# Kernel tuning notes

Hardware: AMD Instinct MI355X
Metric: run time of the kernel (lower is better)

The kernel has to match this reference:

```python
import jax, jax.numpy as jnp
import numpy as np

D = 256          # descriptor_dim
H = 4            # num heads in AttentionPropagation
DH = D // H
SCALE = 0.1      # hparams['scale_factor']
THR = 0.2        # hparams['match_threshold']
NAMES = ['GATs', 'self', 'cross'] * 4


def conv1d(x, w, b):
    # 1x1 Conv1d == per-position matmul. x:[b,c,n] w:[o,c] b:[o]
    return jnp.einsum('oc,bcn->bon', w, x) + b[None, :, None]


def instnorm(x, eps=1e-5):
    # torch InstanceNorm1d (affine=False): normalize over spatial dim per channel
    mu = jnp.mean(x, axis=2, keepdims=True)
    var = jnp.var(x, axis=2, keepdims=True)
    return (x - mu) * jax.lax.rsqrt(var + eps)


def linear_attention(q, k, v):
    # q:[b,dh,h,nq] k,v:[b,dh,h,ns]
    eps = 1e-6
    q = jax.nn.elu(q) + 1.0
    k = jax.nn.elu(k) + 1.0
    m = v.shape[3]
    v = v / m
    KV = jnp.einsum('bdhm,bqhm->bqdh', k, v)
    Z = 1.0 / (jnp.einsum('bdhm,bdh->bhm', q, k.sum(3)) + eps)
    return jnp.einsum('bdhm,bqdh,bhm->bqhm', q, KV, Z) * m


def mha(x, src, pw, pb, mw, mb):
    b, _, nq = x.shape
    ns = src.shape[2]
    q = conv1d(x, pw[0], pb[0]).reshape(b, DH, H, nq)
    k = conv1d(src, pw[1], pb[1]).reshape(b, DH, H, ns)
    v = conv1d(src, pw[2], pb[2]).reshape(b, DH, H, ns)
    o = linear_attention(q, k, v).reshape(b, D, nq)
    return conv1d(o, mw, mb)


def attn_prop(x, src, pw, pb, mw, mb, w1, b1, w2, b2):
    msg = mha(x, src, pw, pb, mw, mb)
    y = jnp.concatenate([x, msg], axis=1)           # [b, 2D, n]
    y = jax.nn.relu(instnorm(conv1d(y, w1, b1)))
    return conv1d(y, w2, b2)


def gat(d2d, d3d, W, a):
    # GraphAttentionLayer (OnePose): include_self=True, additional=False,
    # with_linear_transform=True, concat=True; dropout inactive at eval.
    # d2d:[b,D,n*L] d3d:[b,D,n]
    b, _, n = d3d.shape
    x2 = jnp.transpose(d2d, (0, 2, 1)).reshape(b, n, -1, D)   # [b,n,L,D]
    x3 = jnp.transpose(d3d, (0, 2, 1))                        # [b,n,D]
    x2 = jnp.concatenate([x3[:, :, None, :], x2], axis=2)     # include self -> L+1
    Wh2 = jnp.einsum('bnld,do->bnlo', x2, W)
    Wh3 = jnp.einsum('bnd,do->bno', x3, W)
    e = jax.nn.leaky_relu(
        jnp.einsum('bno,o->bn', Wh3, a[:D])[:, :, None]
        + jnp.einsum('bnlo,o->bnl', Wh2, a[D:]), 0.2)
    att = jax.nn.softmax(e, axis=-1)
    h = jnp.einsum('bnl,bnld->bnd', att, Wh2)
    return jnp.transpose(jax.nn.elu(h), (0, 2, 1))            # [b,D,n]


def gnn_and_scores(dq, d3, d2db, projw, projb, mergew, mergeb,
                   mlp1w, mlp1b, mlp2w, mlp2b, gatW, gata, finw, finb):
    gi = 0
    ai = 0
    for name in NAMES:
        if name == 'GATs':
            d3 = gat(d2db, d3, gatW[gi], gata[gi])
            gi += 1
        else:
            src0, src1 = (d3, dq) if name == 'cross' else (dq, d3)
            p = (projw[ai], projb[ai], mergew[ai], mergeb[ai],
                 mlp1w[ai], mlp1b[ai], mlp2w[ai], mlp2b[ai])
            dq = dq + attn_prop(dq, src0, *p)
            d3 = d3 + attn_prop(d3, src1, *p)
            ai += 1
    mq = conv1d(dq, finw, finb)
    md = conv1d(d3, finw, finb)
    mq = mq / jnp.maximum(jnp.linalg.norm(mq, axis=1, keepdims=True), 1e-12)
    md = md / jnp.maximum(jnp.linalg.norm(md, axis=1, keepdims=True), 1e-12)
    scores = jnp.einsum('bdn,bdm->bnm', mq, md) / SCALE
    conf = jax.nn.softmax(scores, axis=1) * jax.nn.softmax(scores, axis=2)
    return conf


def setup_inputs() -> dict:
    key = jax.random.key(0)
    ks = jax.random.split(key, 16)
    b, n1, n2, L = 2, 3072, 3072, 8
    s = 0.02
    f32 = jnp.float32
    return {
        'desc2d_query': jax.random.normal(ks[0], (b, D, n1), f32),
        'desc3d_db': jax.random.normal(ks[1], (b, D, n2), f32),
        'desc2d_db': jax.random.normal(ks[2], (b, D, n2 * L), f32),
        'projw': jax.random.normal(ks[3], (8, 3, D, D), f32) * s,
        'projb': jnp.zeros((8, 3, D), f32),
        'mergew': jax.random.normal(ks[4], (8, D, D), f32) * s,
        'mergeb': jnp.zeros((8, D), f32),
        'mlp1w': jax.random.normal(ks[5], (8, 2 * D, 2 * D), f32) * s,
        'mlp1b': jnp.zeros((8, 2 * D), f32),
        'mlp2w': jax.random.normal(ks[6], (8, D, 2 * D), f32) * s,
        'mlp2b': jnp.zeros((8, D), f32),
        'gatW': jax.random.normal(ks[7], (4, D, D), f32) * s,
        'gata': jax.random.normal(ks[8], (4, 2 * D), f32) * s,
        'finw': jax.random.normal(ks[9], (D, D), f32) * s,
        'finb': jnp.zeros((D,), f32),
    }


def reference(desc2d_query, desc3d_db, desc2d_db, projw, projb, mergew, mergeb,
              mlp1w, mlp1b, mlp2w, mlp2b, gatW, gata, finw, finb):
    conf = gnn_and_scores(desc2d_query, desc3d_db, desc2d_db, projw, projb,
                          mergew, mergeb, mlp1w, mlp1b, mlp2w, mlp2b,
                          gatW, gata, finw, finb)
    b, n1, n2 = conf.shape
    i0 = jnp.argmax(conf, axis=2)
    m0 = jnp.max(conf, axis=2)
    i1 = jnp.argmax(conf, axis=1)
    m1 = jnp.max(conf, axis=1)
    mutual0 = jnp.arange(n1)[None] == jnp.take_along_axis(i1, i0, axis=1)
    mutual1 = jnp.arange(n2)[None] == jnp.take_along_axis(i0, i1, axis=1)
    ms0 = jnp.where(mutual0, m0, 0.0)
    ms1 = jnp.where(mutual1, jnp.take_along_axis(ms0, i1, axis=1), 0.0)
    valid0 = mutual0 & (ms0 > THR)
    valid1 = mutual1 & jnp.take_along_axis(valid0, i1, axis=1)
    ind0 = jnp.where(valid0, i0, -1)
    ind1 = jnp.where(valid1, i1, -1)
    return (ind0[0], ind1[0], ms0[0], ms1[0], conf)
```

## Files before the change

### kernel.cpp

```cpp
#include <hip/hip_runtime.h>
#include <hip/hip_bf16.h>
#include <math.h>

typedef long long ll;
typedef __attribute__((ext_vector_type(8))) short s8v;
typedef __attribute__((ext_vector_type(4))) float f4v;
typedef __attribute__((address_space(1))) unsigned int gu32;
typedef __attribute__((address_space(3))) unsigned int lu32;

#define NPOS 3072

#define OFF_STF   0LL
#define OFF_STB   3145728LL
#define OFF_QKV   4718592LL
#define OFF_MSG   9437184LL
#define OFF_HID   11010048LL
#define OFF_WBF   14155776LL
#define OFF_PBP   16941056LL
#define OFF_UVEC  17026048LL
#define OFF_E2ALL 17028096LL
#define OFF_PMAX  17300480LL
#define OFF_PSUM  17595392LL
#define OFF_CMAX  17890304LL
#define OFF_CSUM  17896448LL
#define OFF_CAPV  17902592LL
#define OFF_CAPI  17976320LL
#define OFF_I0    18050048LL
#define OFF_M0    18053120LL
#define OFF_I1    18056192LL
#define OFF_M1B   18059264LL
#define OFF_B1C   18583552LL
#define OFF_INAT  18587648LL
#define OFF_SVSQ  18620416LL
#define OFF_KVAT  18632704LL
#define OFF_KSAT  19156992LL
#define ZERO_N    577536LL

__device__ __forceinline__ float b2f(short s) {
  union { unsigned u; float f; } c;
  c.u = ((unsigned)(unsigned short)s) << 16;
  return c.f;
}
__device__ __forceinline__ short f2b(float f) {
  __hip_bfloat16 h = __float2bfloat16(f);
  union { __hip_bfloat16 h; short s; } c; c.h = h; return c.s;
}
__device__ __forceinline__ unsigned pk2(float a, float b) {
  return (unsigned)(unsigned short)f2b(a) | ((unsigned)(unsigned short)f2b(b) << 16);
}
__device__ __forceinline__ float waveSum(float v) {
#pragma unroll
  for (int off = 32; off > 0; off >>= 1) v += __shfl_down(v, off);
  return v;
}
__device__ __forceinline__ void gld16(const short* g, short* l) {
  __builtin_amdgcn_global_load_lds((const gu32*)g, (lu32*)l, 16, 0, 0);
}
template<int N> __device__ __forceinline__ void wvm() {
  asm volatile("s_waitcnt vmcnt(%0)" :: "n"(N) : "memory");
}
__device__ __forceinline__ void wlgk0() {
  asm volatile("s_waitcnt lgkmcnt(0)" ::: "memory");
}

template<int BI, int BJ, int KT, int SMODE>
__global__ __launch_bounds__(256) void bgemm_k(
    const short* __restrict__ A, const short* __restrict__ A2, int KS,
    int lda, int lda2,
    const short* __restrict__ B,
    const float* __restrict__ bias, const float* __restrict__ R,
    float* __restrict__ C, short* __restrict__ C2,
    const float* __restrict__ rs, const float* __restrict__ cs,
    int ldc, float alpha,
    ll aB, ll a2B, ll bB, ll rB, ll cB, ll c2B,
    int za, int zbo, int act, int zand,
    float* __restrict__ sp0, float* __restrict__ sp1, int rsmode)
{
  constexpr int NT = KT / 32;
  constexpr int WI = (BI == 128) ? 2 : 1;
  constexpr int JW = BJ / (4 / WI);
  constexpr int FI = (BI / WI) / 16;
  constexpr int FJ = JW / 16;
  constexpr int SA = BI / 64, SB = BJ / 64;
  constexpr int LPT = SA + SB;
  __shared__ __align__(16) short As[3][BI * 32];
  __shared__ __align__(16) short Bs[3][BJ * 32];
  const int z = blockIdx.z;
  const int zA = (z + za) & zand, zB = (z + zbo) & zand;
  const int j0 = blockIdx.x * BJ, i0 = blockIdx.y * BI;
  const int t = threadIdx.x;
  const int lane = t & 63, w = t >> 6;
  const int wi = (WI == 2) ? (w & 1) * 64 : 0;
  const int wj = (WI == 2) ? (w >> 1) * JW : w * JW;
  const int fr = lane & 15;
  const int cl = lane >> 4;
  const int r4 = cl * 4;

  const short* baseA[SA]; const short* baseA2[SA]; const short* baseB[SB];
  int slA[SA], slB[SB];
  {
    const short* Az = A + (ll)zA * aB;
    const short* A2z = A2 ? A2 + (ll)zA * a2B : nullptr;
    const short* Bz = B + (ll)zB * bB;
#pragma unroll
    for (int i = 0; i < SA; ++i) {
      int cc = t + i * 256;
      int r = cc >> 2;
      int sq = ((cc & 3) ^ ((r >> 1) & 3)) << 3;
      baseA[i] = Az + (ll)(i0 + r) * lda + sq;
      baseA2[i] = A2 ? A2z + (ll)(i0 + r) * lda2 + sq : nullptr;
      slA[i] = cc << 3;
    }
#pragma unroll
    for (int i = 0; i < SB; ++i) {
      int cc = t + i * 256;
      int r = cc >> 2;
      int sq = ((cc & 3) ^ ((r >> 1) & 3)) << 3;
      baseB[i] = Bz + (ll)(j0 + r) * KT + sq;
      slB[i] = cc << 3;
    }
  }
  int offA[FI], offB[FJ];
#pragma unroll
  for (int im = 0; im < FI; ++im) {
    int ra = wi + im * 16 + fr;
    offA[im] = ra * 32 + ((cl ^ ((ra >> 1) & 3)) << 3);
  }
#pragma unroll
  for (int in = 0; in < FJ; ++in) {
    int rb = wj + in * 16 + fr;
    offB[in] = rb * 32 + ((cl ^ ((rb >> 1) & 3)) << 3);
  }

  f4v acc[FI][FJ];
#pragma unroll
  for (int i = 0; i < FI; ++i)
#pragma unroll
    for (int j = 0; j < FJ; ++j) acc[i][j] = (f4v)0.f;

  auto stage = [&](int tile, int bi_) {
    const int k0 = tile * 32;
    short* dA = As[bi_]; short* dB = Bs[bi_];
    if (A2 && k0 >= KS) {
#pragma unroll
      for (int i = 0; i < SA; ++i) gld16(baseA2[i] + (k0 - KS), dA + slA[i]);
    } else {
#pragma unroll
      for (int i = 0; i < SA; ++i) gld16(baseA[i] + k0, dA + slA[i]);
    }
#pragma unroll
    for (int i = 0; i < SB; ++i) gld16(baseB[i] + k0, dB + slB[i]);
  };

  stage(0, 0);
  stage(1, 1);
#pragma unroll
  for (int kt = 0; kt < NT; ++kt) {
    if (kt + 2 < NT) { stage(kt + 2, (kt + 2) % 3); wvm<2 * LPT>(); }
    else if (kt + 1 < NT) { wvm<LPT>(); }
    else { wvm<0>(); }
    __builtin_amdgcn_s_barrier();
    asm volatile("" ::: "memory");
    const short* Ac = As[kt % 3]; const short* Bc = Bs[kt % 3];
    s8v af[FI], bfr[FJ];
#pragma unroll
    for (int im = 0; im < FI; ++im) af[im] = *(const s8v*)(Ac + offA[im]);
#pragma unroll
    for (int in = 0; in < FJ; ++in) bfr[in] = *(const s8v*)(Bc + offB[in]);
#pragma unroll
    for (int im = 0; im < FI; ++im)
#pragma unroll
      for (int in = 0; in < FJ; ++in)
        acc[im][in] = __builtin_amdgcn_mfma_f32_16x16x32_bf16(
            af[im], bfr[in], acc[im][in], 0, 0, 0);
    if (kt + 1 < NT) {
      wlgk0();
      __builtin_amdgcn_s_barrier();
    }
  }

  float* Cz = C ? C + (ll)z * cB : nullptr;
  short* C2z = C2 ? C2 + (ll)z * c2B : nullptr;
  const float* Rz = R ? R + (ll)z * rB : nullptr;
  const float* rsz = rs ? rs + (ll)z * NPOS : nullptr;
  float bv4[FJ], cv4[FJ];
#pragma unroll
  for (int in = 0; in < FJ; ++in) {
    int j = j0 + wj + in * 16 + fr;
    bv4[in] = bias ? bias[j] : 0.f;
    cv4[in] = cs ? cs[(ll)zB * NPOS + j] : 1.f;
    if (rsmode) cv4[in] = 1.f / fmaxf(sqrtf(cv4[in]), 1e-12f);
  }
  float stM[FJ], stS[FJ], stQ[FJ];
#pragma unroll
  for (int in = 0; in < FJ; ++in) { stM[in] = -3.4e38f; stS[in] = 0.f; stQ[in] = 0.f; }

#pragma unroll
  for (int im = 0; im < FI; ++im) {
#pragma unroll
    for (int r = 0; r < 4; ++r) {
      int i = i0 + wi + im * 16 + r4 + r;
      float rsv = rsz ? rsz[i] : 1.f;
      if (rsmode) rsv = 1.f / fmaxf(sqrtf(rsv), 1e-12f);
      int rowo = i * ldc;
      float rq3 = 0.f;
#pragma unroll
      for (int in = 0; in < FJ; ++in) {
        int j = j0 + wj + in * 16 + fr;
        float v = acc[im][in][r] * alpha;
        if (rsz) v = v * rsv * cv4[in];
        v += bv4[in];
        int off = rowo + j;
        if (Rz) v += Rz[off];
        if (act) v = v > 0.f ? v : (expf(v) - 1.f);
        if constexpr (SMODE == 1) {
          float m = stM[in];
          if (v > m) { stS[in] = stS[in] * expf(m - v) + 1.f; stM[in] = v; }
          else stS[in] += expf(v - m);
        }
        if constexpr (SMODE == 2) { stS[in] += v; stQ[in] = fmaf(v, v, stQ[in]); }
        if constexpr (SMODE == 3) rq3 = fmaf(v, v, rq3);
        if (Cz) Cz[off] = v;
        if (C2z) C2z[off] = f2b(v);
      }
      if constexpr (SMODE == 3) {
        rq3 += __shfl_xor(rq3, 1);
        rq3 += __shfl_xor(rq3, 2);
        rq3 += __shfl_xor(rq3, 4);
        rq3 += __shfl_xor(rq3, 8);
        if (fr == 0) atomicAdd(&sp0[(ll)z * NPOS + i], rq3);
      }
    }
  }
  if constexpr (SMODE == 1) {
    const ll totj = (ll)gridDim.x * BJ;
#pragma unroll
    for (int in = 0; in < FJ; ++in) {
      float m = stM[in], s = stS[in];
#pragma unroll
      for (int d = 16; d <= 32; d <<= 1) {
        float mo = __shfl_xor(m, d);
        float so = __shfl_xor(s, d);
        float M = fmaxf(m, mo);
        s = s * expf(m - M) + so * expf(mo - M);
        m = M;
      }
      if (cl == 0) {
        ll o = ((ll)z * gridDim.y + blockIdx.y) * totj + (j0 + wj + in * 16 + fr);
        sp0[o] = m; sp1[o] = s;
      }
    }
  }
  if constexpr (SMODE == 2) {
    const ll totj = (ll)gridDim.x * BJ;
#pragma unroll
    for (int in = 0; in < FJ; ++in) {
      float s = stS[in], q = stQ[in];
      s += __shfl_xor(s, 16); s += __shfl_xor(s, 32);
      q += __shfl_xor(q, 16); q += __shfl_xor(q, 32);
      if (cl == 0) {
        ll o = ((ll)z * totj + (j0 + wj + in * 16 + fr)) * 2;
        atomicAdd(&sp0[o], s);
        atomicAdd(&sp0[o + 1], q);
      }
    }
  }
}

__global__ void zero_k(float* __restrict__ p, int n)
{
  int i = blockIdx.x * 1024 + threadIdx.x * 4;
  if (i < n) *(float4*)(p + i) = make_float4(0.f, 0.f, 0.f, 0.f);
}

__global__ void transpose_in_k(const float* __restrict__ dq, const float* __restrict__ d3,
                               float* __restrict__ stf, short* __restrict__ stb)
{
  __shared__ float tile[64][65];
  int z = blockIdx.z;
  const float* src = (z < 2) ? dq + (ll)z * 786432 : d3 + (ll)(z - 2) * 786432;
  int c0 = blockIdx.y * 64, n0 = blockIdx.x * 64;
  int t = threadIdx.x;
  int nj = t & 63, q = t >> 6;
#pragma unroll
  for (int i = 0; i < 16; ++i) {
    int ci = q + i * 4;
    tile[ci][nj] = src[(ll)(c0 + ci) * NPOS + n0 + nj];
  }
  __syncthreads();
  int cj = t & 63;
#pragma unroll
  for (int i = 0; i < 16; ++i) {
    int ni = q + i * 4;
    float v = tile[cj][ni];
    ll o = (ll)z * 786432 + (ll)(n0 + ni) * 256 + c0 + cj;
    stf[o] = v;
    stb[o] = f2b(v);
  }
}

__global__ void f2b_k(const float* __restrict__ src, short* __restrict__ dst, int n8)
{
  int gi = blockIdx.x * 256 + threadIdx.x;
  if (gi >= n8) return;
  ll e = (ll)gi * 8;
  float4 a = *(const float4*)(src + e);
  float4 b = *(const float4*)(src + e + 4);
  uint4 o;
  o.x = pk2(a.x, a.y); o.y = pk2(a.z, a.w);
  o.z = pk2(b.x, b.y); o.w = pk2(b.z, b.w);
  *(uint4*)(dst + e) = o;
}

__global__ void f2b_split_k(const float* __restrict__ src, short* __restrict__ d1,
                            short* __restrict__ d2)
{
  int gi = blockIdx.x * 256 + threadIdx.x;
  ll e = (ll)gi * 8;
  int k = (int)(e & 511);
  ll row = e >> 9;
  float4 a = *(const float4*)(src + e);
  float4 b = *(const float4*)(src + e + 4);
  uint4 o;
  o.x = pk2(a.x, a.y); o.y = pk2(a.z, a.w);
  o.z = pk2(b.x, b.y); o.w = pk2(b.z, b.w);
  if (k < 256) *(uint4*)(d1 + row * 512 + k) = o;
  else         *(uint4*)(d2 + row * 256 + (k - 256)) = o;
}

__global__ void projw_perm_k(const float* __restrict__ src, short* __restrict__ dst)
{
  int idx = blockIdx.x * 256 + threadIdx.x;
  int c = idx & 255;
  int row = (idx >> 8) % 768;
  int ai = (idx >> 8) / 768;
  int sec = row >> 8;
  int p = row & 255;
  int o = (p & 63) * 4 + (p >> 6);
  dst[idx] = f2b(src[(((ll)ai * 3 + sec) * 256 + o) * 256 + c]);
}

__global__ void pbp_k(const float* __restrict__ pb, float* __restrict__ pbp)
{
  int idx = blockIdx.x * 256 + threadIdx.x;
  int row = idx % 768, ai = idx / 768;
  int sec = row >> 8;
  int p = row & 255;
  int o = (p & 63) * 4 + (p >> 6);
  pbp[idx] = pb[ai * 768 + (sec << 8) + o];
}

__global__ void mergewT_k(const float* __restrict__ src, short* __restrict__ dst)
{
  __shared__ float tile[64][65];
  int ai = blockIdx.z;
  int p0 = blockIdx.x * 64, c0 = blockIdx.y * 64;
  int h = p0 >> 6;
  int t = threadIdx.x;
  int q = t & 63, cq = t >> 6;
#pragma unroll
  for (int i = 0; i < 16; ++i) {
    int cc = cq + i * 4;
    tile[q][cc] = src[(ll)ai * 65536 + (ll)(c0 + cc) * 256 + 4 * q + h];
  }
  __syncthreads();
#pragma unroll
  for (int i = 0; i < 16; ++i) {
    int pi = cq + i * 4;
    dst[((ll)ai * 256 + p0 + pi) * 256 + c0 + q] = f2b(tile[pi][q]);
  }
}

__global__ void biasfold_k(const float* __restrict__ mlp1w, const float* __restrict__ mlp1b,
                           const float* __restrict__ mergeb, float* __restrict__ b1c)
{
  int b = blockIdx.x;
  int ai = b >> 3, o0 = (b & 7) * 64;
  int t = threadIdx.x;
  int w = t >> 6, lane = t & 63;
  float4 mb = *(const float4*)(mergeb + ai * 256 + lane * 4);
#pragma unroll
  for (int ol = 0; ol < 16; ++ol) {
    int o = o0 + w * 16 + ol;
    float4 wv = *(const float4*)(mlp1w + ((ll)(ai * 512 + o)) * 512 + 256 + lane * 4);
    float s = wv.x * mb.x + wv.y * mb.y + wv.z * mb.z + wv.w * mb.w;
    s = waveSum(s);
    if (lane == 0) b1c[ai * 512 + o] = mlp1b[ai * 512 + o] + s;
  }
}

__global__ void gatw_t_k(const float* __restrict__ src, short* __restrict__ dst)
{
  __shared__ float tile[64][65];
  int gi = blockIdx.z;
  int d0 = blockIdx.x * 64, o0 = blockIdx.y * 64;
  int t = threadIdx.x;
  int nj = t & 63, q = t >> 6;
#pragma unroll
  for (int i = 0; i < 16; ++i) {
    int di = q + i * 4;
    tile[di][nj] = src[(ll)gi * 65536 + (ll)(d0 + di) * 256 + o0 + nj];
  }
  __syncthreads();
#pragma unroll
  for (int i = 0; i < 16; ++i) {
    int oi = q + i * 4;
    dst[(ll)gi * 65536 + (ll)(o0 + oi) * 256 + d0 + nj] = f2b(tile[nj][oi]);
  }
}

__global__ void gat_prep_k(const float* __restrict__ gatW, const float* __restrict__ gata,
                           float* __restrict__ uvec)
{
  int gi = blockIdx.x; int d = threadIdx.x;
  const float* W = gatW + (ll)gi * 65536;
  const float* a = gata + gi * 512;
  float u0 = 0.f, u1 = 0.f;
  for (int o = 0; o < 256; o += 4) {
    float4 w4 = *(const float4*)(W + d * 256 + o);
    float4 a4 = *(const float4*)(a + o);
    float4 b4 = *(const float4*)(a + 256 + o);
    u0 += w4.x * a4.x + w4.y * a4.y + w4.z * a4.z + w4.w * a4.w;
    u1 += w4.x * b4.x + w4.y * b4.y + w4.z * b4.z + w4.w * b4.w;
  }
  uvec[gi * 512 + d] = u0;
  uvec[gi * 512 + 256 + d] = u1;
}

__global__ void e2all_k(const float* __restrict__ d2db, const float* __restrict__ uvec,
                        float* __restrict__ e2all)
{
  __shared__ float us[1024];
  int t = threadIdx.x;
  for (int idx = t; idx < 1024; idx += 256)
    us[idx] = uvec[(idx >> 8) * 512 + 256 + (idx & 255)];
  __syncthreads();
  int m = blockIdx.x * 256 + t;
  int b = blockIdx.y;
  const float* xb = d2db + (ll)b * 6291456;
  float a[4] = {};
  for (int c = 0; c < 256; ++c) {
    float v = xb[(ll)c * 24576 + m];
#pragma unroll
    for (int g = 0; g < 4; ++g) a[g] = fmaf(v, us[g * 256 + c], a[g]);
  }
#pragma unroll
  for (int g = 0; g < 4; ++g) e2all[((ll)g * 2 + b) * 24576 + m] = a[g];
}

__global__ __launch_bounds__(256) void gat_g_k(
    const short* __restrict__ stb, const float* __restrict__ d2db,
    const float* __restrict__ uvec, const float* __restrict__ e2all,
    short* __restrict__ g, int gi)
{
  __shared__ float ush[512];
  __shared__ float attw[576];
  __shared__ float gtile[64 * 69];
  const int n0 = blockIdx.x * 64, c0 = blockIdx.y * 64, b = blockIdx.z;
  const int t = threadIdx.x;
  for (int idx = t; idx < 512; idx += 256) ush[idx] = uvec[gi * 512 + idx];
  __syncthreads();
  {
    const int q = t & 3, pl = t >> 2;
    const int n = n0 + pl;
    const short* xr = stb + (ll)(2 + b) * 786432 + (ll)n * 256 + q * 64;
    float a0 = 0.f, a1 = 0.f;
#pragma unroll
    for (int i = 0; i < 8; ++i) {
      s8v v8 = *(const s8v*)(xr + i * 8);
#pragma unroll
      for (int j = 0; j < 8; ++j) {
        float v = b2f(v8[j]);
        a0 = fmaf(v, ush[q * 64 + i * 8 + j], a0);
        a1 = fmaf(v, ush[256 + q * 64 + i * 8 + j], a1);
      }
    }
    a0 += __shfl_xor(a0, 1); a0 += __shfl_xor(a0, 2);
    a1 += __shfl_xor(a1, 1); a1 += __shfl_xor(a1, 2);
    if (q == 0) {
      float e[9];
      e[0] = a0 + a1;
      const float* e2b = e2all + ((ll)gi * 2 + b) * 24576 + (ll)n * 8;
#pragma unroll
      for (int l = 0; l < 8; ++l) e[l + 1] = a0 + e2b[l];
      float mx = -3.4e38f;
#pragma unroll
      for (int l = 0; l < 9; ++l) {
        e[l] = e[l] >= 0.f ? e[l] : 0.2f * e[l];
        mx = fmaxf(mx, e[l]);
      }
      float s = 0.f;
#pragma unroll
      for (int l = 0; l < 9; ++l) { e[l] = expf(e[l] - mx); s += e[l]; }
      float inv = 1.f / s;
#pragma unroll
      for (int l = 0; l < 9; ++l) attw[pl * 9 + l] = e[l] * inv;
    }
  }
  __syncthreads();
  const int nl = t >> 2, l2 = (t & 3) * 2;
  for (int cc = 0; cc < 64; ++cc) {
    const float* src = d2db + ((ll)b * 256 + c0 + cc) * 24576 + (ll)n0 * 8;
    float2 v = *(const float2*)(src + t * 2);
    float p = v.x * attw[nl * 9 + 1 + l2] + v.y * attw[nl * 9 + 2 + l2];
    p += __shfl_xor(p, 1);
    p += __shfl_xor(p, 2);
    if ((t & 3) == 0) gtile[nl * 69 + cc] = p;
  }
  __syncthreads();
#pragma unroll
  for (int i = 0; i < 4; ++i) {
    int n = (t >> 4) + i * 16;
    int cp = (t & 15) * 4;
    float at0 = attw[n * 9];
    const short* dr = stb + (ll)(2 + b) * 786432 + (ll)(n0 + n) * 256 + c0 + cp;
    uint2 dv = *(const uint2*)dr;
    float d0 = b2f((short)(dv.x & 0xffff)), d1 = b2f((short)(dv.x >> 16));
    float d2 = b2f((short)(dv.y & 0xffff)), d3v = b2f((short)(dv.y >> 16));
    uint2 ov;
    ov.x = pk2(gtile[n * 69 + cp] + at0 * d0, gtile[n * 69 + cp + 1] + at0 * d1);
    ov.y = pk2(gtile[n * 69 + cp + 2] + at0 * d2, gtile[n * 69 + cp + 3] + at0 * d3v);
    *(uint2*)(g + (ll)b * 786432 + (ll)(n0 + n) * 256 + c0 + cp) = ov;
  }
}

__global__ __launch_bounds__(256) void kv_partial_k(
    const short* __restrict__ qkv, float* __restrict__ kvat, float* __restrict__ ksat)
{
  __shared__ float ks[32][66];
  __shared__ float vs[32][66];
  const int p = blockIdx.x, h = blockIdx.y, z = blockIdx.z;
  const short* base = qkv + (ll)z * 2359296;
  const int t = threadIdx.x;
  const int tq = (t >> 4) * 4, tk = (t & 15) * 4;
  const int ml = t >> 3, d8 = (t & 7) * 8;
  float acc[4][4] = {};
  float ksl = 0.f;
  for (int sub = 0; sub < 8; ++sub) {
    int m0 = p * 256 + sub * 32;
    {
      const short* kr = base + (ll)(m0 + ml) * 768 + 256 + h * 64 + d8;
      s8v k8 = *(const s8v*)kr;
      s8v v8 = *(const s8v*)(kr + 256);
#pragma unroll
      for (int j = 0; j < 8; ++j) {
        float kvv = b2f(k8[j]);
        ks[ml][d8 + j] = kvv > 0.f ? kvv + 1.f : expf(kvv);
        vs[ml][d8 + j] = b2f(v8[j]);
      }
    }
    __syncthreads();
#pragma unroll 8
    for (int mm = 0; mm < 32; ++mm) {
      float vv[4], kk[4];
#pragma unroll
      for (int i = 0; i < 4; ++i) { vv[i] = vs[mm][tq + i]; kk[i] = ks[mm][tk + i]; }
#pragma unroll
      for (int i = 0; i < 4; ++i)
#pragma unroll
        for (int j = 0; j < 4; ++j)
          acc[i][j] = fmaf(vv[i], kk[j], acc[i][j]);
    }
    if (t < 64) {
#pragma unroll 8
      for (int mm = 0; mm < 32; ++mm) ksl += ks[mm][t];
    }
    __syncthreads();
  }
  float* kvz = kvat + ((ll)z * 4 + h) * 4096;
#pragma unroll
  for (int i = 0; i < 4; ++i)
#pragma unroll
    for (int j = 0; j < 4; ++j)
      atomicAdd(&kvz[(tk + j) * 64 + tq + i], acc[i][j]);
  if (t < 64) atomicAdd(&ksat[(z * 4 + h) * 64 + t], ksl);
}

__global__ __launch_bounds__(256) void attn_out_k(
    const short* __restrict__ qkv, const float* __restrict__ kv,
    const float* __restrict__ ksum, short* __restrict__ obuf)
{
  __shared__ float qt[64][67];
  __shared__ float kvT[64][66];
  __shared__ float zsh[64];
  __shared__ float kss[64];
  const int n0 = blockIdx.x * 64, h = blockIdx.y, z = blockIdx.z;
  const int t = threadIdx.x;
  {
    int nl = t >> 3, d8 = (t & 7) * 8;
    const short* qr0 = qkv + (ll)z * 2359296 + (ll)(n0 + nl) * 768 + h * 64 + d8;
#pragma unroll
    for (int i = 0; i < 2; ++i) {
      const short* qr = qr0 + (ll)i * 32 * 768;
      s8v q8 = *(const s8v*)qr;
#pragma unroll
      for (int j = 0; j < 8; ++j) {
        float q = b2f(q8[j]);
        qt[nl + i * 32][d8 + j] = q > 0.f ? q + 1.f : expf(q);
      }
    }
  }
  {
    const float* kvb = kv + (ll)(z * 4 + h) * 4096;
#pragma unroll
    for (int i = 0; i < 16; ++i) {
      int idx = t + i * 256;
      kvT[idx >> 6][idx & 63] = kvb[idx];
    }
  }
  if (t < 64) kss[t] = ksum[(z * 4 + h) * 64 + t];
  __syncthreads();
  if (t < 64) {
    float s = 0.f;
    for (int d = 0; d < 64; ++d) s = fmaf(qt[t][d], kss[d], s);
    zsh[t] = 1.f / (s + 1e-6f);
  }
  __syncthreads();
  const int tn = t >> 4, tj = t & 15;
  float acc[4][4] = {};
  for (int d = 0; d < 64; ++d) {
    float av[4], bv[4];
#pragma unroll
    for (int i = 0; i < 4; ++i) av[i] = qt[tn * 4 + i][d];
    *(float4*)bv = *(const float4*)&kvT[d][tj * 4];
#pragma unroll
    for (int i = 0; i < 4; ++i)
#pragma unroll
      for (int j = 0; j < 4; ++j)
        acc[i][j] = fmaf(av[i], bv[j], acc[i][j]);
  }
#pragma unroll
  for (int i = 0; i < 4; ++i) {
    int n = n0 + tn * 4 + i;
    float zv = zsh[tn * 4 + i];
    uint2 o;
    o.x = pk2(acc[i][0] * zv, acc[i][1] * zv);
    o.y = pk2(acc[i][2] * zv, acc[i][3] * zv);
    *(uint2*)(obuf + (ll)z * 786432 + (ll)n * 256 + h * 64 + tj * 4) = o;
  }
}

__global__ void in_apply_k(short* __restrict__ hid, const float* __restrict__ inat)
{
  int z = blockIdx.z, cg = blockIdx.y, nc = blockIdx.x;
  int t = threadIdx.x;
  int c = cg * 64 + (t & 63);
  float2 sq = *(const float2*)(inat + ((ll)(z * 512 + c) << 1));
  float mu = sq.x * (1.f / NPOS);
  float var = sq.y * (1.f / NPOS) - mu * mu;
  float rsig = rsqrtf(fmaxf(var, 0.f) + 1e-5f);
  short* base = hid + (ll)z * 1572864 + (ll)(nc * 384 + (t >> 6)) * 512 + c;
#pragma unroll 4
  for (int i = 0; i < 96; ++i) {
    float v = (b2f(base[(ll)i * 2048]) - mu) * rsig;
    base[(ll)i * 2048] = f2b(v > 0.f ? v : 0.f);
  }
}

__global__ void colstat_comb_k(const float* __restrict__ pmax, const float* __restrict__ psum,
                               float* __restrict__ cmax, float* __restrict__ csum)
{
  int m = blockIdx.x * 256 + threadIdx.x; int b = blockIdx.y;
  float M = -3.4e38f;
  for (int c = 0; c < 48; ++c) M = fmaxf(M, pmax[((ll)b * 48 + c) * NPOS + m]);
  float s = 0.f;
  for (int c = 0; c < 48; ++c)
    s += psum[((ll)b * 48 + c) * NPOS + m] * expf(pmax[((ll)b * 48 + c) * NPOS + m] - M);
  cmax[b * NPOS + m] = M; csum[b * NPOS + m] = s;
}

__global__ __launch_bounds__(256) void rowfix_k(
    float* __restrict__ S, const float* __restrict__ cmax, const float* __restrict__ csum,
    int* __restrict__ i0, float* __restrict__ m0)
{
  int n = blockIdx.x, b = blockIdx.y, t = threadIdx.x;
  float* row = S + (ll)b * 9437184 + (ll)n * NPOS;
  __shared__ float red[4];
  float v[12];
  float mx = -3.4e38f;
#pragma unroll
  for (int i = 0; i < 12; ++i) { v[i] = row[t + i * 256]; mx = fmaxf(mx, v[i]); }
#pragma unroll
  for (int off = 32; off > 0; off >>= 1) mx = fmaxf(mx, __shfl_down(mx, off));
  if ((t & 63) == 0) red[t >> 6] = mx;
  __syncthreads();
  float rm = fmaxf(fmaxf(red[0], red[1]), fmaxf(red[2], red[3]));
  __syncthreads();
  float s = 0.f;
#pragma unroll
  for (int i = 0; i < 12; ++i) s += expf(v[i] - rm);
  s = waveSum(s);
  if ((t & 63) == 0) red[t >> 6] = s;
  __syncthreads();
  float irs = 1.f / (red[0] + red[1] + red[2] + red[3]);
  float bv = -1.f; int bi = 0;
#pragma unroll
  for (int i = 0; i < 12; ++i) {
    int m = t + i * 256;
    float f = expf(2.f * v[i] - rm - cmax[b * NPOS + m]) * irs / csum[b * NPOS + m];
    row[m] = f;
    if (f > bv) { bv = f; bi = m; }
  }
  if (b == 0) {
#pragma unroll
    for (int off = 32; off > 0; off >>= 1) {
      float ov = __shfl_down(bv, off);
      int oi = __shfl_down(bi, off);
      if (ov > bv || (ov == bv && oi < bi)) { bv = ov; bi = oi; }
    }
    __shared__ float rv[4]; __shared__ int ri[4];
    if ((t & 63) == 0) { rv[t >> 6] = bv; ri[t >> 6] = bi; }
    __syncthreads();
    if (t == 0) {
      for (int w = 1; w < 4; ++w)
        if (rv[w] > bv || (rv[w] == bv && ri[w] < bi)) { bv = rv[w]; bi = ri[w]; }
      i0[n] = bi; m0[n] = bv;
    }
  }
}

__global__ void colamax_part_k(const float* __restrict__ Cf,
                               float* __restrict__ capv, int* __restrict__ capi)
{
  int m = blockIdx.x * 256 + threadIdx.x;
  int n0 = blockIdx.y * 128;
  float bv = -1.f; int bi = 0;
  for (int n = n0; n < n0 + 128; ++n) {
    float f = Cf[(ll)n * NPOS + m];
    if (f > bv) { bv = f; bi = n; }
  }
  capv[blockIdx.y * NPOS + m] = bv;
  capi[blockIdx.y * NPOS + m] = bi;
}

__global__ void colamax_comb_k(const float* __restrict__ capv, const int* __restrict__ capi,
                               int* __restrict__ i1)
{
  int m = blockIdx.x * 256 + threadIdx.x;
  float bv = -1.f; int bi = 0;
  for (int c = 0; c < 24; ++c) {
    float v = capv[c * NPOS + m];
    if (v > bv) { bv = v; bi = capi[c * NPOS + m]; }
  }
  i1[m] = bi;
}

__global__ void match0_k(const int* __restrict__ i0, const float* __restrict__ m0,
                         const int* __restrict__ i1, float* __restrict__ out)
{
  int n = blockIdx.x * 256 + threadIdx.x;
  int j = i0[n];
  bool mut = (i1[j] == n);
  float ms0 = mut ? m0[n] : 0.f;
  bool valid = mut && (ms0 > 0.2f);
  out[n] = valid ? (float)j : -1.f;
  out[6144 + n] = ms0;
}

__global__ void match1_k(const int* __restrict__ i0, const int* __restrict__ i1,
                         float* __restrict__ out)
{
  int m = blockIdx.x * 256 + threadIdx.x;
  int j = i1[m];
  bool mut = (i0[j] == m);
  float ms0v = out[6144 + j];
  float ind0v = out[j];
  float ms1 = mut ? ms0v : 0.f;
  bool valid1 = mut && (ind0v >= 0.f);
  out[3072 + m] = valid1 ? (float)j : -1.f;
  out[9216 + m] = ms1;
}

extern "C" void kernel_launch(void* const* d_in, const int* in_sizes, int n_in,
                              void* d_out, int out_size, void* d_ws, size_t ws_size,
                              hipStream_t stream)
{
  const float* desc2dq = (const float*)d_in[0];
  const float* desc3db = (const float*)d_in[1];
  const float* desc2db = (const float*)d_in[2];
  const float* projw = (const float*)d_in[3];
  const float* projb = (const float*)d_in[4];
  const float* mergew = (const float*)d_in[5];
  const float* mergeb = (const float*)d_in[6];
  const float* mlp1w = (const float*)d_in[7];
  const float* mlp1b = (const float*)d_in[8];
  const float* mlp2w = (const float*)d_in[9];
  const float* mlp2b = (const float*)d_in[10];
  const float* gatW = (const float*)d_in[11];
  const float* gata = (const float*)d_in[12];
  const float* finw = (const float*)d_in[13];
  const float* finb = (const float*)d_in[14];

  float* ws = (float*)d_ws;
  float* out = (float*)d_out;

  float* stf = ws + OFF_STF;
  short* stb = (short*)(ws + OFF_STB);
  short* qkv = (short*)(ws + OFF_QKV);
  short* msg = (short*)(ws + OFF_MSG);
  short* obuf = msg;
  short* hid = (short*)(ws + OFF_HID);
  short* wbf = (short*)(ws + OFF_WBF);
  short* projw_bf = wbf;
  short* mergewT_bf = wbf + 1572864;
  short* mlp1c_bf = wbf + 2097152;
  short* mlp2w_bf = wbf + 4194304;
  short* gatwT_bf = wbf + 5242880;
  short* finw_bf = wbf + 5505024;
  float* pbp = ws + OFF_PBP;
  float* uvec = ws + OFF_UVEC;
  float* e2all = ws + OFF_E2ALL;
  float* pmax = ws + OFF_PMAX;
  float* psum = ws + OFF_PSUM;
  float* cmax = ws + OFF_CMAX;
  float* csum = ws + OFF_CSUM;
  float* capv = ws + OFF_CAPV;
  int* capi = (int*)(ws + OFF_CAPI);
  int* i0 = (int*)(ws + OFF_I0);
  float* m0 = ws + OFF_M0;
  int* i1 = (int*)(ws + OFF_I1);
  short* m1b_bf = (short*)(ws + OFF_M1B);
  float* b1c = ws + OFF_B1C;
  float* inat = ws + OFF_INAT;
  float* svsq = ws + OFF_SVSQ;
  float* kvat = ws + OFF_KVAT;
  float* ksat = ws + OFF_KSAT;
  short* finbf = msg;

  zero_k<<<564, 256, 0, stream>>>(inat, (int)ZERO_N);
  transpose_in_k<<<dim3(48, 4, 4), 256, 0, stream>>>(desc2dq, desc3db, stf, stb);
  projw_perm_k<<<6144, 256, 0, stream>>>(projw, projw_bf);
  pbp_k<<<24, 256, 0, stream>>>(projb, pbp);
  mergewT_k<<<dim3(4, 4, 8), 256, 0, stream>>>(mergew, mergewT_bf);
  f2b_split_k<<<1024, 256, 0, stream>>>(mlp1w, mlp1c_bf, m1b_bf);
  f2b_k<<<512, 256, 0, stream>>>(mlp2w, mlp2w_bf, 131072);
  gatw_t_k<<<dim3(4, 4, 4), 256, 0, stream>>>(gatW, gatwT_bf);
  f2b_k<<<32, 256, 0, stream>>>(finw, finw_bf, 8192);
  biasfold_k<<<64, 256, 0, stream>>>(mlp1w, mlp1b, mergeb, b1c);
  bgemm_k<64, 128, 256, 0><<<dim3(2, 8, 8), 256, 0, stream>>>(
      m1b_bf, nullptr, 0, 256, 0, mergewT_bf, nullptr, nullptr,
      nullptr, mlp1c_bf + 256, nullptr, nullptr,
      512, 1.f, 131072, 0, 65536, 0, 0, 262144, 0, 0, 0, 7,
      nullptr, nullptr, 0);
  gat_prep_k<<<4, 256, 0, stream>>>(gatW, gata, uvec);
  e2all_k<<<dim3(96, 2), 256, 0, stream>>>(desc2db, uvec, e2all);

  auto attn_layer = [&](int ai, int cross) {
    const short* pw = projw_bf + (ll)ai * 196608;
    const float* pb = pbp + (ll)ai * 768;
    if (!cross) {
      bgemm_k<64, 128, 256, 0><<<dim3(6, 48, 4), 256, 0, stream>>>(
          stb, nullptr, 0, 256, 0, pw, pb, nullptr, nullptr, qkv, nullptr, nullptr,
          768, 1.f, 786432, 0, 0, 0, 0, 2359296, 0, 0, 0, 3,
          nullptr, nullptr, 0);
    } else {
      bgemm_k<64, 64, 256, 0><<<dim3(4, 48, 4), 256, 0, stream>>>(
          stb, nullptr, 0, 256, 0, pw, pb, nullptr, nullptr, qkv, nullptr, nullptr,
          768, 1.f, 786432, 0, 0, 0, 0, 2359296, 0, 0, 0, 3,
          nullptr, nullptr, 0);
      bgemm_k<64, 128, 256, 0><<<dim3(4, 48, 4), 256, 0, stream>>>(
          stb, nullptr, 0, 256, 0, pw + 65536, pb + 256, nullptr, nullptr, qkv + 256,
          nullptr, nullptr,
          768, 1.f, 786432, 0, 0, 0, 0, 2359296, 2, 0, 0, 3,
          nullptr, nullptr, 0);
    }
    kv_partial_k<<<dim3(12, 4, 4), 256, 0, stream>>>(
        qkv, kvat + (ll)ai * 65536, ksat + (ll)ai * 1024);
    attn_out_k<<<dim3(48, 4, 4), 256, 0, stream>>>(
        qkv, kvat + (ll)ai * 65536, ksat + (ll)ai * 1024, obuf);
    bgemm_k<64, 128, 512, 2><<<dim3(4, 48, 4), 256, 0, stream>>>(
        stb, obuf, 256, 256, 256, mlp1c_bf + (ll)ai * 262144, b1c + (ll)ai * 512,
        nullptr, nullptr, hid, nullptr, nullptr,
        512, 1.f, 786432, 786432, 0, 0, 0, 1572864, 0, 0, 0, 3,
        inat + (ll)ai * 4096, nullptr, 0);
    in_apply_k<<<dim3(8, 8, 4), 256, 0, stream>>>(hid, inat + (ll)ai * 4096);
    bgemm_k<64, 64, 512, 0><<<dim3(4, 48, 4), 256, 0, stream>>>(
        hid, nullptr, 0, 512, 0, mlp2w_bf + (ll)ai * 131072, mlp2b + (ll)ai * 256,
        stf, stf, stb, nullptr, nullptr,
        256, 1.f, 1572864, 0, 0, 786432, 786432, 786432, 0, 0, 0, 3,
        nullptr, nullptr, 0);
  };

  auto gat_layer = [&](int gi) {
    gat_g_k<<<dim3(48, 4, 2), 256, 0, stream>>>(stb, desc2db, uvec, e2all, obuf, gi);
    bgemm_k<64, 64, 256, 0><<<dim3(4, 48, 2), 256, 0, stream>>>(
        obuf, nullptr, 0, 256, 0, gatwT_bf + (ll)gi * 65536, nullptr, nullptr,
        stf + (ll)2 * 786432, stb + (ll)2 * 786432, nullptr, nullptr,
        256, 1.f, 786432, 0, 0, 0, 786432, 786432, 0, 0, 1, 3,
        nullptr, nullptr, 0);
  };

  int ai = 0, gi = 0;
  for (int r = 0; r < 4; ++r) {
    gat_layer(gi); gi++;
    attn_layer(ai, 0); ai++;
    attn_layer(ai, 1); ai++;
  }

  bgemm_k<64, 64, 256, 3><<<dim3(4, 48, 4), 256, 0, stream>>>(
      stb, nullptr, 0, 256, 0, finw_bf, finb, nullptr, nullptr, finbf, nullptr, nullptr,
      256, 1.f, 786432, 0, 0, 0, 0, 786432, 0, 0, 0, 3,
      svsq, nullptr, 0);

  float* conf = out + 12288;
  bgemm_k<64, 128, 256, 1><<<dim3(24, 48, 2), 256, 0, stream>>>(
      finbf, nullptr, 0, 256, 0, finbf, nullptr, nullptr, conf, nullptr, svsq, svsq,
      3072, 10.f, 786432, 0, 786432, 0, 9437184, 0, 0, 2, 0, 3,
      pmax, psum, 1);

  colstat_comb_k<<<dim3(12, 2), 256, 0, stream>>>(pmax, psum, cmax, csum);
  rowfix_k<<<dim3(NPOS, 2), 256, 0, stream>>>(conf, cmax, csum, i0, m0);
  colamax_part_k<<<dim3(12, 24), 256, 0, stream>>>(conf, capv, capi);
  colamax_comb_k<<<12, 256, 0, stream>>>(capv, capi, i1);
  match0_k<<<12, 256, 0, stream>>>(i0, m0, i1, out);
  match1_k<<<12, 256, 0, stream>>>(i0, i1, out);
}
```

Baseline: 1.523 ms.

## Merge cross-attention QKV GEMMs into one launch and use single-barrier pipeline

Adds per-block-column A-batch offset parameters (jq, zaq) so the cross-attention Q projection and the K/V projections, which read different batch slices, run in a single 6x48x4 GEMM launch instead of two. The k-loop is also reordered to use one barrier per iteration: it waits on loads and LDS, barriers, then issues the next prefetch before computing. The aim is to cut a kernel launch per cross layer and one barrier per k-step, at the cost of issuing the prefetch after the barrier, which gives it less time to overlap.

Result: slower. 1.556 ms (+2.1%).

```diff
diff --git a/kernel.cpp b/kernel.cpp
--- a/kernel.cpp
+++ b/kernel.cpp
@@ -73,7 +73,7 @@
     const float* __restrict__ rs, const float* __restrict__ cs,
     int ldc, float alpha,
     ll aB, ll a2B, ll bB, ll rB, ll cB, ll c2B,
-    int za, int zbo, int act, int zand,
+    int za, int zbo, int act, int zand, int jq, int zaq,
     float* __restrict__ sp0, float* __restrict__ sp1, int rsmode)
 {
   constexpr int NT = KT / 32;
@@ -86,7 +86,8 @@
   __shared__ __align__(16) short As[3][BI * 32];
   __shared__ __align__(16) short Bs[3][BJ * 32];
   const int z = blockIdx.z;
-  const int zA = (z + za) & zand, zB = (z + zbo) & zand;
+  const int zae = (jq > 0 && (int)blockIdx.x < jq) ? zaq : za;
+  const int zA = (z + zae) & zand, zB = (z + zbo) & zand;
   const int j0 = blockIdx.x * BJ, i0 = blockIdx.y * BI;
   const int t = threadIdx.x;
   const int lane = t & 63, w = t >> 6;
@@ -156,11 +157,11 @@
   stage(1, 1);
 #pragma unroll
   for (int kt = 0; kt < NT; ++kt) {
-    if (kt + 2 < NT) { stage(kt + 2, (kt + 2) % 3); wvm<2 * LPT>(); }
-    else if (kt + 1 < NT) { wvm<LPT>(); }
-    else { wvm<0>(); }
+    if (kt + 1 < NT) { wvm<LPT>(); } else { wvm<0>(); }
+    wlgk0();
     __builtin_amdgcn_s_barrier();
     asm volatile("" ::: "memory");
+    if (kt + 2 < NT) stage(kt + 2, (kt + 2) % 3);
     const short* Ac = As[kt % 3]; const short* Bc = Bs[kt % 3];
     s8v af[FI], bfr[FJ];
 #pragma unroll
@@ -173,10 +174,6 @@
       for (int in = 0; in < FJ; ++in)
         acc[im][in] = __builtin_amdgcn_mfma_f32_16x16x32_bf16(
             af[im], bfr[in], acc[im][in], 0, 0, 0);
-    if (kt + 1 < NT) {
-      wlgk0();
-      __builtin_amdgcn_s_barrier();
-    }
   }
 
   float* Cz = C ? C + (ll)z * cB : nullptr;
@@ -840,7 +837,7 @@
   bgemm_k<64, 128, 256, 0><<<dim3(2, 8, 8), 256, 0, stream>>>(
       m1b_bf, nullptr, 0, 256, 0, mergewT_bf, nullptr, nullptr,
       nullptr, mlp1c_bf + 256, nullptr, nullptr,
-      512, 1.f, 131072, 0, 65536, 0, 0, 262144, 0, 0, 0, 7,
+      512, 1.f, 131072, 0, 65536, 0, 0, 262144, 0, 0, 0, 7, 0, 0,
       nullptr, nullptr, 0);
   gat_prep_k<<<4, 256, 0, stream>>>(gatW, gata, uvec);
   e2all_k<<<dim3(96, 2), 256, 0, stream>>>(desc2db, uvec, e2all);
@@ -848,22 +845,11 @@
   auto attn_layer = [&](int ai, int cross) {
     const short* pw = projw_bf + (ll)ai * 196608;
     const float* pb = pbp + (ll)ai * 768;
-    if (!cross) {
-      bgemm_k<64, 128, 256, 0><<<dim3(6, 48, 4), 256, 0, stream>>>(
-          stb, nullptr, 0, 256, 0, pw, pb, nullptr, nullptr, qkv, nullptr, nullptr,
-          768, 1.f, 786432, 0, 0, 0, 0, 2359296, 0, 0, 0, 3,
-          nullptr, nullptr, 0);
-    } else {
-      bgemm_k<64, 64, 256, 0><<<dim3(4, 48, 4), 256, 0, stream>>>(
-          stb, nullptr, 0, 256, 0, pw, pb, nullptr, nullptr, qkv, nullptr, nullptr,
-          768, 1.f, 786432, 0, 0, 0, 0, 2359296, 0, 0, 0, 3,
-          nullptr, nullptr, 0);
-      bgemm_k<64, 128, 256, 0><<<dim3(4, 48, 4), 256, 0, stream>>>(
-          stb, nullptr, 0, 256, 0, pw + 65536, pb + 256, nullptr, nullptr, qkv + 256,
-          nullptr, nullptr,
-          768, 1.f, 786432, 0, 0, 0, 0, 2359296, 2, 0, 0, 3,
-          nullptr, nullptr, 0);
-    }
+    bgemm_k<64, 128, 256, 0><<<dim3(6, 48, 4), 256, 0, stream>>>(
+        stb, nullptr, 0, 256, 0, pw, pb, nullptr, nullptr, qkv, nullptr, nullptr,
+        768, 1.f, 786432, 0, 0, 0, 0, 2359296, cross ? 2 : 0, 0, 0, 3,
+        cross ? 2 : 0, 0,
+        nullptr, nullptr, 0);
     kv_partial_k<<<dim3(12, 4, 4), 256, 0, stream>>>(
         qkv, kvat + (ll)ai * 65536, ksat + (ll)ai * 1024);
     attn_out_k<<<dim3(48, 4, 4), 256, 0, stream>>>(
@@ -871,13 +857,13 @@
     bgemm_k<64, 128, 512, 2><<<dim3(4, 48, 4), 256, 0, stream>>>(
         stb, obuf, 256, 256, 256, mlp1c_bf + (ll)ai * 262144, b1c + (ll)ai * 512,
         nullptr, nullptr, hid, nullptr, nullptr,
-        512, 1.f, 786432, 786432, 0, 0, 0, 1572864, 0, 0, 0, 3,
+        512, 1.f, 786432, 786432, 0, 0, 0, 1572864, 0, 0, 0, 3, 0, 0,
         inat + (ll)ai * 4096, nullptr, 0);
     in_apply_k<<<dim3(8, 8, 4), 256, 0, stream>>>(hid, inat + (ll)ai * 4096);
     bgemm_k<64, 64, 512, 0><<<dim3(4, 48, 4), 256, 0, stream>>>(
         hid, nullptr, 0, 512, 0, mlp2w_bf + (ll)ai * 131072, mlp2b + (ll)ai * 256,
         stf, stf, stb, nullptr, nullptr,
-        256, 1.f, 1572864, 0, 0, 786432, 786432, 786432, 0, 0, 0, 3,
+        256, 1.f, 1572864, 0, 0, 786432, 786432, 786432, 0, 0, 0, 3, 0, 0,
         nullptr, nullptr, 0);
   };
 
@@ -886,7 +872,7 @@
     bgemm_k<64, 64, 256, 0><<<dim3(4, 48, 2), 256, 0, stream>>>(
         obuf, nullptr, 0, 256, 0, gatwT_bf + (ll)gi * 65536, nullptr, nullptr,
         stf + (ll)2 * 786432, stb + (ll)2 * 786432, nullptr, nullptr,
-        256, 1.f, 786432, 0, 0, 0, 786432, 786432, 0, 0, 1, 3,
+        256, 1.f, 786432, 0, 0, 0, 786432, 786432, 0, 0, 1, 3, 0, 0,
         nullptr, nullptr, 0);
   };
 
@@ -899,13 +885,13 @@
 
   bgemm_k<64, 64, 256, 3><<<dim3(4, 48, 4), 256, 0, stream>>>(
       stb, nullptr, 0, 256, 0, finw_bf, finb, nullptr, nullptr, finbf, nullptr, nullptr,
-      256, 1.f, 786432, 0, 0, 0, 0, 786432, 0, 0, 0, 3,
+      256, 1.f, 786432, 0, 0, 0, 0, 786432, 0, 0, 0, 3, 0, 0,
       svsq, nullptr, 0);
 
   float* conf = out + 12288;
   bgemm_k<64, 128, 256, 1><<<dim3(24, 48, 2), 256, 0, stream>>>(
       finbf, nullptr, 0, 256, 0, finbf, nullptr, nullptr, conf, nullptr, svsq, svsq,
-      3072, 10.f, 786432, 0, 786432, 0, 9437184, 0, 0, 2, 0, 3,
+      3072, 10.f, 786432, 0, 786432, 0, 9437184, 0, 0, 2, 0, 3, 0, 0,
       pmax, psum, 1);
 
   colstat_comb_k<<<dim3(12, 2), 256, 0, stream>>>(pmax, psum, cmax, csum);
```
